# Optimization experiments

Hardware: AMD Instinct MI355X
Metric: run time of the kernel (lower is better)

The kernel has to match this reference:

```python
import jax, jax.numpy as jnp
import numpy as np

N_GROUPS = 32
EPS = 1e-5
N_HEADS = 8
D_K = 64


def setup_inputs() -> dict:
    key = jax.random.key(0)
    ks = jax.random.split(key, 4)
    B, C, H, W = 16, 512, 32, 32
    x = jax.random.normal(ks[0], (B, C, H, W), dtype=jnp.float32)
    gn_w = jnp.ones((C,), dtype=jnp.float32)
    gn_b = jnp.zeros((C,), dtype=jnp.float32)
    proj_w = jax.random.normal(ks[1], (3 * C, C), dtype=jnp.float32) * (C ** -0.5)
    proj_b = jnp.zeros((3 * C,), dtype=jnp.float32)
    out_w = jax.random.normal(ks[2], (C, C), dtype=jnp.float32) * (C ** -0.5)
    out_b = jnp.zeros((C,), dtype=jnp.float32)
    return {"x": x, "gn_w": gn_w, "gn_b": gn_b, "proj_w": proj_w,
            "proj_b": proj_b, "out_w": out_w, "out_b": out_b}


def _group_norm(x, w, b):
    B, C, H, W = x.shape
    xg = x.reshape(B, N_GROUPS, C // N_GROUPS, H, W)
    mean = xg.mean(axis=(2, 3, 4), keepdims=True)
    var = xg.var(axis=(2, 3, 4), keepdims=True)
    xn = (xg - mean) * jax.lax.rsqrt(var + EPS)
    xn = xn.reshape(B, C, H, W)
    return xn * w[None, :, None, None] + b[None, :, None, None]


def reference(x, gn_w, gn_b, proj_w, proj_b, out_w, out_b):
    B, C, H, W = x.shape
    S = H * W
    scale = D_K ** -0.25  # applied to both q and k, as in the original
    h = _group_norm(x, gn_w, gn_b).reshape(B, C, S).transpose(0, 2, 1)  # [B,S,C]
    qkv = h @ proj_w.T + proj_b  # [B,S,3C]
    qkv = qkv.reshape(B, S, N_HEADS, 3 * D_K)
    q, k, v = jnp.split(qkv, 3, axis=-1)  # each [B,S,H,D]
    attn = jnp.einsum('bihd,bjhd->bijh', q * scale, k * scale)  # [B,S,S,Hd]
    attn = jax.nn.softmax(attn, axis=2)
    res = jnp.einsum('bijh,bjhd->bihd', attn, v).reshape(B, S, N_HEADS * D_K)
    res = res @ out_w.T + out_b  # [B,S,C]
    res = res.transpose(0, 2, 1).reshape(B, C, H, W)
    return res + x
```

## Files before the change

### kernel.cpp

```cpp
#include <hip/hip_runtime.h>
#include <stdint.h>

typedef unsigned short u16;
typedef __attribute__((ext_vector_type(8))) short bf16x8;
typedef __attribute__((ext_vector_type(4))) short bf16x4;
typedef __attribute__((ext_vector_type(4))) float f32x4;
typedef __attribute__((ext_vector_type(4))) unsigned short u16x4;

#define GLD16(gp, lp) __builtin_amdgcn_global_load_lds( \
    (__attribute__((address_space(1))) void*)(void*)(gp), \
    (__attribute__((address_space(3))) void*)(void*)(lp), 16, 0, 0)

__device__ __forceinline__ u16 f2b(float f) {
  union { float f; unsigned u; } v; v.f = f;
  unsigned r = v.u + 0x7FFFu + ((v.u >> 16) & 1u);
  return (u16)(r >> 16);
}

__device__ __forceinline__ float fexp2(float x) {
#if __has_builtin(__builtin_amdgcn_exp2f)
  return __builtin_amdgcn_exp2f(x);
#else
  return exp2f(x);
#endif
}

__global__ __launch_bounds__(256) void gncvt_kernel(const float* __restrict__ x,
                                                    const float* __restrict__ gw,
                                                    const float* __restrict__ gb,
                                                    u16* __restrict__ h,
                                                    const float* __restrict__ wq_f,
                                                    const float* __restrict__ wo_f,
                                                    u16* __restrict__ wq,
                                                    u16* __restrict__ wo) {
  if (blockIdx.x >= 512) {
    int i = (blockIdx.x - 512) * 256 + threadIdx.x;
    const float* src; u16* dst; int j;
    if (i < 196608) { src = wq_f; dst = wq; j = i; }
    else            { src = wo_f; dst = wo; j = i - 196608; }
    const float4 f = ((const float4*)src)[j];
    u16x4 r; r[0] = f2b(f.x); r[1] = f2b(f.y); r[2] = f2b(f.z); r[3] = f2b(f.w);
    *(u16x4*)(dst + (size_t)j * 4) = r;
    return;
  }
  const int b = blockIdx.x >> 5, g = blockIdx.x & 31;
  const float* xg = x + ((size_t)(b * 512 + g * 16)) * 1024;
  const int tid = threadIdx.x;
  float4 vals[16];
  float s = 0.f, ss = 0.f;
#pragma unroll
  for (int j = 0; j < 16; j++) {
    const float4 v = ((const float4*)xg)[j * 256 + tid];
    vals[j] = v;
    s  += (v.x + v.y) + (v.z + v.w);
    ss += (v.x * v.x + v.y * v.y) + (v.z * v.z + v.w * v.w);
  }
#pragma unroll
  for (int off = 32; off; off >>= 1) { s += __shfl_down(s, off); ss += __shfl_down(ss, off); }
  __shared__ float red[8];
  const int wid = tid >> 6, lane = tid & 63;
  if (lane == 0) { red[wid] = s; red[4 + wid] = ss; }
  __syncthreads();
  if (tid == 0) {
    float S = red[0] + red[1] + red[2] + red[3];
    float SS = red[4] + red[5] + red[6] + red[7];
    float mean = S * (1.f / 16384.f);
    float var = SS * (1.f / 16384.f) - mean * mean;
    red[0] = mean; red[1] = rsqrtf(var + 1e-5f);
  }
  __syncthreads();
  const float mean = red[0], rs = red[1];
  float sc[16], bi[16];
#pragma unroll
  for (int c = 0; c < 16; c++) { sc[c] = gw[g * 16 + c] * rs; bi[c] = gb[g * 16 + c]; }
  u16* dst = h + ((size_t)(b * 32 + g) * 1024 + 4 * tid) * 16;
#pragma unroll
  for (int e = 0; e < 4; e++) {
    u16 row[16];
#pragma unroll
    for (int j = 0; j < 16; j++) {
      const float v = (e == 0) ? vals[j].x : (e == 1) ? vals[j].y : (e == 2) ? vals[j].z : vals[j].w;
      row[j] = f2b((v - mean) * sc[j] + bi[j]);
    }
    *(bf16x8*)(dst + e * 16) = *(bf16x8*)&row[0];
    *(bf16x8*)(dst + e * 16 + 8) = *(bf16x8*)&row[8];
  }
}

__global__ __launch_bounds__(512, 2) void qkv_gemm(const u16* __restrict__ h,
                                                   const u16* __restrict__ w,
                                                   const float* __restrict__ bias,
                                                   u16* __restrict__ q,
                                                   u16* __restrict__ k,
                                                   u16* __restrict__ v) {
  __shared__ u16 As[2][256 * 64];
  __shared__ u16 Bs[2][256 * 64];
  const int bm = blockIdx.x;
  const int bn = blockIdx.y;
  const int tid = threadIdx.x, lane = tid & 63, wid = tid >> 6;
  const int wm = wid & 1, wn = wid >> 1;
  const int c15 = lane & 15, quad = lane >> 4;
  const int sw = c15 & 7;
  const int b = bm >> 2;
  const int sp0 = (bm & 3) * 256;

  const int t8 = tid >> 3;
  const int lc = (tid & 7) ^ (t8 & 7);
  const u16* pA = h + (size_t)b * 524288 + (size_t)(lc >> 1) * 16384
                + (size_t)(sp0 + t8) * 16 + (lc & 1) * 8;
  const u16* pB = w + (size_t)(bn * 256 + t8) * 512 + lc * 8;

  const f32x4 fz = {0.f, 0.f, 0.f, 0.f};
  f32x4 acc[8][4];
#pragma unroll
  for (int i = 0; i < 8; i++)
#pragma unroll
    for (int j = 0; j < 4; j++) acc[i][j] = fz;

#pragma unroll
  for (int i = 0; i < 4; i++) {
    GLD16(pA + (size_t)i * 1024, &As[0][(i * 512 + tid) * 8]);
    GLD16(pB + (size_t)i * 32768, &Bs[0][(i * 512 + tid) * 8]);
  }
  asm volatile("s_waitcnt vmcnt(0)" ::: "memory");
  __builtin_amdgcn_s_barrier();
  __builtin_amdgcn_sched_barrier(0);

  for (int kt = 0; kt < 8; ++kt) {
    const int cb = kt & 1, db = cb ^ 1;
    if (kt < 7) {
#pragma unroll
      for (int i = 0; i < 4; i++) {
        GLD16(pA + (size_t)(kt + 1) * 65536 + (size_t)i * 1024, &As[db][(i * 512 + tid) * 8]);
        GLD16(pB + (size_t)(kt + 1) * 64 + (size_t)i * 32768, &Bs[db][(i * 512 + tid) * 8]);
      }
      __builtin_amdgcn_sched_barrier(0);
    }
    bf16x8 bfx[2][4];
#pragma unroll
    for (int kk = 0; kk < 2; kk++) {
      const int kc = ((kk * 4 + quad) ^ sw) * 8;
#pragma unroll
      for (int ni = 0; ni < 4; ni++)
        bfx[kk][ni] = *(const bf16x8*)&Bs[cb][(wn * 64 + ni * 16 + c15) * 64 + kc];
    }
#pragma unroll
    for (int ph = 0; ph < 2; ph++) {
      bf16x8 af[2][4];
#pragma unroll
      for (int kk = 0; kk < 2; kk++) {
        const int kc = ((kk * 4 + quad) ^ sw) * 8;
#pragma unroll
        for (int mi = 0; mi < 4; mi++)
          af[kk][mi] = *(const bf16x8*)&As[cb][(wm * 128 + ph * 64 + mi * 16 + c15) * 64 + kc];
      }
      __builtin_amdgcn_s_setprio(1);
#pragma unroll
      for (int kk = 0; kk < 2; kk++)
#pragma unroll
        for (int mi = 0; mi < 4; mi++)
#pragma unroll
          for (int ni = 0; ni < 4; ni++)
            acc[ph * 4 + mi][ni] = __builtin_amdgcn_mfma_f32_16x16x32_bf16(af[kk][mi], bfx[kk][ni], acc[ph * 4 + mi][ni], 0, 0, 0);
      __builtin_amdgcn_s_setprio(0);
    }
    asm volatile("s_waitcnt vmcnt(0)" ::: "memory");
    __builtin_amdgcn_s_barrier();
    __builtin_amdgcn_sched_barrier(0);
  }

  const float qscale = 0.51006972f;
  const float kscale = 0.35355339059327373f;
  const int quad4 = quad << 2;
#pragma unroll
  for (int mi = 0; mi < 8; mi++) {
    const int sp = sp0 + wm * 128 + mi * 16 + quad4;
#pragma unroll
    for (int ni = 0; ni < 4; ni++) {
      const int n = bn * 256 + wn * 64 + ni * 16 + c15;
      const int head = n / 192;
      const int rr = n - head * 192;
      const float bi = bias[n];
      const int d = rr & 63;
      if (rr < 128) {
        u16* dst = (rr < 64) ? q : k;
        const float sc = (rr < 64) ? qscale : kscale;
        dst += ((size_t)(b * 8 + head) * 1024 + sp) * 64 + d;
#pragma unroll
        for (int r = 0; r < 4; r++)
          dst[(size_t)r * 64] = f2b((acc[mi][ni][r] + bi) * sc);
      } else {
        u16x4 pk;
#pragma unroll
        for (int r = 0; r < 4; r++) pk[r] = f2b(acc[mi][ni][r] + bi);
        *(u16x4*)(v + ((size_t)(b * 8 + head) * 64 + d) * 1024 + sp) = pk;
      }
    }
  }
}

__global__ __launch_bounds__(512) void attn_kernel(const u16* __restrict__ q,
                                                   const u16* __restrict__ k,
                                                   const u16* __restrict__ vT,
                                                   u16* __restrict__ o) {
  __shared__ u16 Ks[2][64 * 64];
  __shared__ u16 Vs[2][64 * 64];
  const int bh = blockIdx.x;
  const int qb = blockIdx.y;
  const int tid = threadIdx.x, lane = tid & 63, wid = tid >> 6;
  const u16* Q = q + (size_t)bh * 1024 * 64;
  const u16* K = k + (size_t)bh * 1024 * 64;
  const u16* V = vT + (size_t)bh * 64 * 1024;
  const int qrow0 = qb * 256 + wid * 32;
  const int c15 = lane & 15, quad = lane >> 4;
  const int sw = c15 & 7;
  const int srow = tid >> 3;
  const int u8g  = tid & 7;
  const int s7 = srow & 7;
  const int kld = srow * 64 + ((u8g ^ s7) * 8);
  const int ve = 4 * (u8g >> 2) + 2 * (u8g & 1);
  const int vc = ((u8g >> 1) & 1) * 4;
  const int vld0 = srow * 64 + ((ve ^ s7) * 8) + vc;
  const int vld1 = srow * 64 + (((ve + 1) ^ s7) * 8) + vc;

  bf16x8 qf[2][2];
#pragma unroll
  for (int kk = 0; kk < 2; kk++)
#pragma unroll
    for (int ni = 0; ni < 2; ni++)
      qf[kk][ni] = *(const bf16x8*)(Q + (size_t)(qrow0 + ni * 16 + c15) * 64 + kk * 32 + quad * 8);

  const f32x4 fz = {0.f, 0.f, 0.f, 0.f};
  const float Mshift = 14.4269504089f;
  const f32x4 fm = {-Mshift, -Mshift, -Mshift, -Mshift};
  f32x4 oaccT[4][2];
#pragma unroll
  for (int i = 0; i < 4; i++)
#pragma unroll
    for (int j = 0; j < 2; j++) oaccT[i][j] = fz;
  float lsum[2] = {0.f, 0.f};

  bf16x8 kr, vr;
  kr = *(const bf16x8*)(K + (size_t)srow * 64 + u8g * 8);
  vr = *(const bf16x8*)(V + (size_t)srow * 1024 + u8g * 8);
  {
    u16* Kd = Ks[0]; u16* Vd = Vs[0];
    *(bf16x8*)&Kd[kld] = kr;
    union { bf16x4 h[2]; bf16x8 v; } a; a.v = vr;
    *(bf16x4*)&Vd[vld0] = a.h[0];
    *(bf16x4*)&Vd[vld1] = a.h[1];
  }
  kr = *(const bf16x8*)(K + (size_t)(64 + srow) * 64 + u8g * 8);
  vr = *(const bf16x8*)(V + (size_t)srow * 1024 + 64 + u8g * 8);

  for (int kt = 0; kt < 16; ++kt) {
    __syncthreads();
    const int cur = kt & 1, alt = cur ^ 1;
    if (kt < 15) {
      u16* Kd = Ks[alt]; u16* Vd = Vs[alt];
      *(bf16x8*)&Kd[kld] = kr;
      union { bf16x4 h[2]; bf16x8 v; } a; a.v = vr;
      *(bf16x4*)&Vd[vld0] = a.h[0];
      *(bf16x4*)&Vd[vld1] = a.h[1];
      const int pk2 = (kt + 2) & 15;
      kr = *(const bf16x8*)(K + ((size_t)pk2 * 64 + srow) * 64 + u8g * 8);
      vr = *(const bf16x8*)(V + (size_t)srow * 1024 + pk2 * 64 + u8g * 8);
    }
    const u16* Kc = Ks[cur];
    const u16* Vc = Vs[cur];

    f32x4 sacc[4][2];
#pragma unroll
    for (int i = 0; i < 4; i++)
#pragma unroll
      for (int j = 0; j < 2; j++) sacc[i][j] = fm;
#pragma unroll
    for (int kk = 0; kk < 2; kk++) {
      bf16x8 af[4];
#pragma unroll
      for (int mi = 0; mi < 4; mi++)
        af[mi] = *(const bf16x8*)&Kc[(mi * 16 + c15) * 64 + (((kk * 4 + quad) ^ sw) * 8)];
      __builtin_amdgcn_s_setprio(1);
#pragma unroll
      for (int mi = 0; mi < 4; mi++)
#pragma unroll
        for (int ni = 0; ni < 2; ni++)
          sacc[mi][ni] = __builtin_amdgcn_mfma_f32_16x16x32_bf16(af[mi], qf[kk][ni], sacc[mi][ni], 0, 0, 0);
      __builtin_amdgcn_s_setprio(0);
    }

    unsigned pkd[4][2][2];
#pragma unroll
    for (int ni = 0; ni < 2; ni++) {
      float ls = 0.f;
#pragma unroll
      for (int mi = 0; mi < 4; mi++) {
        unsigned pu[4];
#pragma unroll
        for (int r = 0; r < 4; r++) {
          const float p = fexp2(sacc[mi][ni][r]);
          ls += p;
          union { float f; unsigned u; } c; c.f = p;
          pu[r] = c.u;
        }
        pkd[mi][ni][0] = __builtin_amdgcn_perm(pu[1], pu[0], 0x07060302u);
        pkd[mi][ni][1] = __builtin_amdgcn_perm(pu[3], pu[2], 0x07060302u);
      }
      lsum[ni] += ls;
    }

#pragma unroll
    for (int mg = 0; mg < 2; mg++) {
      union { unsigned u[4]; bf16x8 v; } bb[2];
#pragma unroll
      for (int ni = 0; ni < 2; ni++) {
        bb[ni].u[0] = pkd[2 * mg][ni][0];     bb[ni].u[1] = pkd[2 * mg][ni][1];
        bb[ni].u[2] = pkd[2 * mg + 1][ni][0]; bb[ni].u[3] = pkd[2 * mg + 1][ni][1];
      }
      bf16x8 aa[4];
#pragma unroll
      for (int nd = 0; nd < 4; nd++)
        aa[nd] = *(const bf16x8*)&Vc[(nd * 16 + c15) * 64 + (((mg * 4 + quad) ^ sw) * 8)];
      __builtin_amdgcn_s_setprio(1);
#pragma unroll
      for (int nd = 0; nd < 4; nd++)
#pragma unroll
        for (int ni = 0; ni < 2; ni++)
          oaccT[nd][ni] = __builtin_amdgcn_mfma_f32_16x16x32_bf16(aa[nd], bb[ni].v, oaccT[nd][ni], 0, 0, 0);
      __builtin_amdgcn_s_setprio(0);
    }
  }

  float iv[2];
#pragma unroll
  for (int ni = 0; ni < 2; ni++) {
    float l = lsum[ni];
    l += __shfl_xor(l, 16);
    l += __shfl_xor(l, 32);
    iv[ni] = 1.f / l;
  }
  const int b = bh >> 3, hh = bh & 7;
#pragma unroll
  for (int ni = 0; ni < 2; ni++) {
    const int row = qrow0 + ni * 16 + c15;
#pragma unroll
    for (int nd = 0; nd < 4; nd++) {
      u16x4 pk4;
#pragma unroll
      for (int r = 0; r < 4; r++) pk4[r] = f2b(oaccT[nd][ni][r] * iv[ni]);
      *(u16x4*)(o + ((size_t)b * 1024 + row) * 512 + hh * 64 + nd * 16 + quad * 4) = pk4;
    }
  }
}

__global__ __launch_bounds__(256) void out_gemm(const u16* __restrict__ attn,
                                                const u16* __restrict__ wo,
                                                const float* __restrict__ ob,
                                                const float* __restrict__ x,
                                                float* __restrict__ out) {
  __shared__ u16 As[128 * 32];
  __shared__ u16 Bs[128 * 32];
  const int b = blockIdx.z;
  const int bm = blockIdx.x;
  const int bn = blockIdx.y;
  const int tid = threadIdx.x, lane = tid & 63, wid = tid >> 6;
  const int wm = wid & 1, wn = wid >> 1;
  const u16* gA = attn + ((size_t)b * 1024 + bm * 128) * 512;
  const u16* gB = wo + (size_t)bn * 128 * 512;

  const f32x4 fz = {0.f, 0.f, 0.f, 0.f};
  f32x4 acc[4][4];
#pragma unroll
  for (int i = 0; i < 4; i++)
#pragma unroll
    for (int j = 0; j < 4; j++) acc[i][j] = fz;

  const int r0 = lane >> 2;
  const int ch8 = (lane & 3) * 8;

  for (int kt = 0; kt < 16; ++kt) {
    __syncthreads();
#pragma unroll
    for (int j = 0; j < 2; ++j) {
      const int idx = wid * 2 + j;
      const int row = idx * 16 + r0;
      GLD16(gA + (size_t)row * 512 + kt * 32 + ch8, &As[idx * 512 + lane * 8]);
      GLD16(gB + (size_t)row * 512 + kt * 32 + ch8, &Bs[idx * 512 + lane * 8]);
    }
    __syncthreads();
    bf16x8 af[4], bf[4];
#pragma unroll
    for (int mi = 0; mi < 4; mi++)
      af[mi] = *(const bf16x8*)&As[(wm * 64 + mi * 16 + (lane & 15)) * 32 + (lane >> 4) * 8];
#pragma unroll
    for (int ni = 0; ni < 4; ni++)
      bf[ni] = *(const bf16x8*)&Bs[(wn * 64 + ni * 16 + (lane & 15)) * 32 + (lane >> 4) * 8];
#pragma unroll
    for (int mi = 0; mi < 4; mi++)
#pragma unroll
      for (int ni = 0; ni < 4; ni++)
        acc[mi][ni] = __builtin_amdgcn_mfma_f32_16x16x32_bf16(af[mi], bf[ni], acc[mi][ni], 0, 0, 0);
  }

  const int quad4 = (lane >> 4) << 2;
  const int c15_ = lane & 15;
#pragma unroll
  for (int mi = 0; mi < 4; mi++) {
    const int m = bm * 128 + wm * 64 + mi * 16 + quad4;
#pragma unroll
    for (int ni = 0; ni < 4; ni++) {
      const int c = bn * 128 + wn * 64 + ni * 16 + c15_;
      const float bo = ob[c];
      const size_t idx = ((size_t)b * 512 + c) * 1024 + m;
      const float4 xv = *(const float4*)(x + idx);
      float4 ov;
      ov.x = acc[mi][ni][0] + bo + xv.x;
      ov.y = acc[mi][ni][1] + bo + xv.y;
      ov.z = acc[mi][ni][2] + bo + xv.z;
      ov.w = acc[mi][ni][3] + bo + xv.w;
      *(float4*)(out + idx) = ov;
    }
  }
}

extern "C" void kernel_launch(void* const* d_in, const int* in_sizes, int n_in,
                              void* d_out, int out_size, void* d_ws, size_t ws_size,
                              hipStream_t stream) {
  const float* x      = (const float*)d_in[0];
  const float* gn_w   = (const float*)d_in[1];
  const float* gn_b   = (const float*)d_in[2];
  const float* proj_w = (const float*)d_in[3];
  const float* proj_b = (const float*)d_in[4];
  const float* out_w  = (const float*)d_in[5];
  const float* out_b  = (const float*)d_in[6];
  float* out = (float*)d_out;

  char* p = (char*)d_ws;
  u16* h    = (u16*)p; p += (size_t)16 * 1024 * 512 * 2;
  u16* q    = (u16*)p; p += (size_t)16 * 8 * 1024 * 64 * 2;
  u16* k    = (u16*)p; p += (size_t)16 * 8 * 1024 * 64 * 2;
  u16* v    = (u16*)p; p += (size_t)16 * 8 * 1024 * 64 * 2;
  u16* attn = (u16*)p; p += (size_t)16 * 1024 * 512 * 2;
  u16* wq   = (u16*)p; p += (size_t)1536 * 512 * 2;
  u16* wo   = (u16*)p; p += (size_t)512 * 512 * 2;

  gncvt_kernel<<<1536, 256, 0, stream>>>(x, gn_w, gn_b, h, proj_w, out_w, wq, wo);
  qkv_gemm<<<dim3(64, 6), 512, 0, stream>>>(h, wq, proj_b, q, k, v);
  attn_kernel<<<dim3(128, 4), 512, 0, stream>>>(q, k, v, attn);
  out_gemm<<<dim3(8, 4, 16), 256, 0, stream>>>(attn, wo, out_b, x, out);
}
```

Before: 204.1 us.

## Pre-tile h and QKV weights into swizzled K-tiles; shrink QKV GEMM tile for occupancy

The group-norm kernel and the weight conversion now write h and the projection weights directly in a pre-tiled, XOR-swizzled [tile][32-wide K] layout, so each GEMM K-step can be loaded with contiguous 16-byte global-to-LDS copies. The QKV GEMM tile drops from 256x256x64 to 256x96x32, which uses far less LDS, allows 4 blocks per CU, and raises the grid from 384 to 1024 blocks to fill the GPU better. The cost is lower per-block data reuse, more K iterations with a barrier each, and 16 rather than 8 pipeline steps.

```diff
diff --git a/kernel.cpp b/kernel.cpp
--- a/kernel.cpp
+++ b/kernel.cpp
@@ -24,6 +24,7 @@
   return exp2f(x);
 #endif
 }
+
 
 __global__ __launch_bounds__(256) void gncvt_kernel(const float* __restrict__ x,
                                                     const float* __restrict__ gw,
@@ -35,12 +36,20 @@
                                                     u16* __restrict__ wo) {
   if (blockIdx.x >= 512) {
     int i = (blockIdx.x - 512) * 256 + threadIdx.x;
-    const float* src; u16* dst; int j;
-    if (i < 196608) { src = wq_f; dst = wq; j = i; }
-    else            { src = wo_f; dst = wo; j = i - 196608; }
-    const float4 f = ((const float4*)src)[j];
-    u16x4 r; r[0] = f2b(f.x); r[1] = f2b(f.y); r[2] = f2b(f.z); r[3] = f2b(f.w);
-    *(u16x4*)(dst + (size_t)j * 4) = r;
+    if (i < 196608) {
+      const float4 f = ((const float4*)wq_f)[i];
+      const int n = i >> 7, c0 = (i & 127) * 4;
+      const int nt = n / 96, r = n - nt * 96;
+      const int kt = c0 >> 5, c8 = (c0 >> 3) & 3, wi = c0 & 7;
+      const int sel = (r >> 1) & 3;
+      u16x4 rr; rr[0] = f2b(f.x); rr[1] = f2b(f.y); rr[2] = f2b(f.z); rr[3] = f2b(f.w);
+      *(u16x4*)(wq + (size_t)(nt * 16 + kt) * 3072 + r * 32 + ((c8 ^ sel) * 8) + wi) = rr;
+    } else {
+      int j = i - 196608;
+      const float4 f = ((const float4*)wo_f)[j];
+      u16x4 rr; rr[0] = f2b(f.x); rr[1] = f2b(f.y); rr[2] = f2b(f.z); rr[3] = f2b(f.w);
+      *(u16x4*)(wo + (size_t)j * 4) = rr;
+    }
     return;
   }
   const int b = blockIdx.x >> 5, g = blockIdx.x & 31;
@@ -73,97 +82,80 @@
   float sc[16], bi[16];
 #pragma unroll
   for (int c = 0; c < 16; c++) { sc[c] = gw[g * 16 + c] * rs; bi[c] = gb[g * 16 + c]; }
-  u16* dst = h + ((size_t)(b * 32 + g) * 1024 + 4 * tid) * 16;
+  const int mt = b * 4 + (tid >> 6);
+  const int kt = g >> 1, c8a = (g & 1) * 2;
+  u16* base = h + (size_t)(mt * 16 + kt) * 8192;
 #pragma unroll
   for (int e = 0; e < 4; e++) {
+    const int r = (tid & 63) * 4 + e;
+    const int sel = (r >> 1) & 3;
     u16 row[16];
 #pragma unroll
     for (int j = 0; j < 16; j++) {
       const float v = (e == 0) ? vals[j].x : (e == 1) ? vals[j].y : (e == 2) ? vals[j].z : vals[j].w;
       row[j] = f2b((v - mean) * sc[j] + bi[j]);
     }
-    *(bf16x8*)(dst + e * 16) = *(bf16x8*)&row[0];
-    *(bf16x8*)(dst + e * 16 + 8) = *(bf16x8*)&row[8];
-  }
-}
-
-__global__ __launch_bounds__(512, 2) void qkv_gemm(const u16* __restrict__ h,
+    *(bf16x8*)(base + r * 32 + ((c8a ^ sel) * 8)) = *(bf16x8*)&row[0];
+    *(bf16x8*)(base + r * 32 + (((c8a + 1) ^ sel) * 8)) = *(bf16x8*)&row[8];
+  }
+}
+
+__global__ __launch_bounds__(512, 4) void qkv_gemm(const u16* __restrict__ h,
                                                    const u16* __restrict__ w,
                                                    const float* __restrict__ bias,
                                                    u16* __restrict__ q,
                                                    u16* __restrict__ k,
                                                    u16* __restrict__ v) {
-  __shared__ u16 As[2][256 * 64];
-  __shared__ u16 Bs[2][256 * 64];
+  __shared__ u16 As[2][8192];
+  __shared__ u16 Bs[2][3072];
   const int bm = blockIdx.x;
   const int bn = blockIdx.y;
   const int tid = threadIdx.x, lane = tid & 63, wid = tid >> 6;
-  const int wm = wid & 1, wn = wid >> 1;
+  const int wm = wid >> 1, wn = wid & 1;
   const int c15 = lane & 15, quad = lane >> 4;
-  const int sw = c15 & 7;
-  const int b = bm >> 2;
-  const int sp0 = (bm & 3) * 256;
-
-  const int t8 = tid >> 3;
-  const int lc = (tid & 7) ^ (t8 & 7);
-  const u16* pA = h + (size_t)b * 524288 + (size_t)(lc >> 1) * 16384
-                + (size_t)(sp0 + t8) * 16 + (lc & 1) * 8;
-  const u16* pB = w + (size_t)(bn * 256 + t8) * 512 + lc * 8;
+  const int kc = ((quad ^ ((c15 >> 1) & 3)) * 8);
+
+  const u16* pA = h + (size_t)bm * 16 * 8192 + (size_t)tid * 8;
+  const u16* pB = w + (size_t)bn * 16 * 3072 + (size_t)tid * 8;
+  const bool doB = (tid < 384);
 
   const f32x4 fz = {0.f, 0.f, 0.f, 0.f};
-  f32x4 acc[8][4];
-#pragma unroll
-  for (int i = 0; i < 8; i++)
-#pragma unroll
-    for (int j = 0; j < 4; j++) acc[i][j] = fz;
-
-#pragma unroll
-  for (int i = 0; i < 4; i++) {
-    GLD16(pA + (size_t)i * 1024, &As[0][(i * 512 + tid) * 8]);
-    GLD16(pB + (size_t)i * 32768, &Bs[0][(i * 512 + tid) * 8]);
-  }
+  f32x4 acc[4][3];
+#pragma unroll
+  for (int i = 0; i < 4; i++)
+#pragma unroll
+    for (int j = 0; j < 3; j++) acc[i][j] = fz;
+
+  GLD16(pA, &As[0][tid * 8]);
+  GLD16(pA + 4096, &As[0][4096 + tid * 8]);
+  if (doB) GLD16(pB, &Bs[0][tid * 8]);
   asm volatile("s_waitcnt vmcnt(0)" ::: "memory");
   __builtin_amdgcn_s_barrier();
   __builtin_amdgcn_sched_barrier(0);
 
-  for (int kt = 0; kt < 8; ++kt) {
+  for (int kt = 0; kt < 16; ++kt) {
     const int cb = kt & 1, db = cb ^ 1;
-    if (kt < 7) {
-#pragma unroll
-      for (int i = 0; i < 4; i++) {
-        GLD16(pA + (size_t)(kt + 1) * 65536 + (size_t)i * 1024, &As[db][(i * 512 + tid) * 8]);
-        GLD16(pB + (size_t)(kt + 1) * 64 + (size_t)i * 32768, &Bs[db][(i * 512 + tid) * 8]);
-      }
+    if (kt < 15) {
+      const u16* nA = pA + (size_t)(kt + 1) * 8192;
+      GLD16(nA, &As[db][tid * 8]);
+      GLD16(nA + 4096, &As[db][4096 + tid * 8]);
+      if (doB) GLD16(pB + (size_t)(kt + 1) * 3072, &Bs[db][tid * 8]);
       __builtin_amdgcn_sched_barrier(0);
     }
-    bf16x8 bfx[2][4];
-#pragma unroll
-    for (int kk = 0; kk < 2; kk++) {
-      const int kc = ((kk * 4 + quad) ^ sw) * 8;
-#pragma unroll
-      for (int ni = 0; ni < 4; ni++)
-        bfx[kk][ni] = *(const bf16x8*)&Bs[cb][(wn * 64 + ni * 16 + c15) * 64 + kc];
-    }
-#pragma unroll
-    for (int ph = 0; ph < 2; ph++) {
-      bf16x8 af[2][4];
-#pragma unroll
-      for (int kk = 0; kk < 2; kk++) {
-        const int kc = ((kk * 4 + quad) ^ sw) * 8;
-#pragma unroll
-        for (int mi = 0; mi < 4; mi++)
-          af[kk][mi] = *(const bf16x8*)&As[cb][(wm * 128 + ph * 64 + mi * 16 + c15) * 64 + kc];
-      }
-      __builtin_amdgcn_s_setprio(1);
-#pragma unroll
-      for (int kk = 0; kk < 2; kk++)
-#pragma unroll
-        for (int mi = 0; mi < 4; mi++)
-#pragma unroll
-          for (int ni = 0; ni < 4; ni++)
-            acc[ph * 4 + mi][ni] = __builtin_amdgcn_mfma_f32_16x16x32_bf16(af[kk][mi], bfx[kk][ni], acc[ph * 4 + mi][ni], 0, 0, 0);
-      __builtin_amdgcn_s_setprio(0);
-    }
+    bf16x8 af[4], bf[3];
+#pragma unroll
+    for (int mi = 0; mi < 4; mi++)
+      af[mi] = *(const bf16x8*)&As[cb][(wm * 64 + mi * 16 + c15) * 32 + kc];
+#pragma unroll
+    for (int ni = 0; ni < 3; ni++)
+      bf[ni] = *(const bf16x8*)&Bs[cb][(wn * 48 + ni * 16 + c15) * 32 + kc];
+    __builtin_amdgcn_s_setprio(1);
+#pragma unroll
+    for (int mi = 0; mi < 4; mi++)
+#pragma unroll
+      for (int ni = 0; ni < 3; ni++)
+        acc[mi][ni] = __builtin_amdgcn_mfma_f32_16x16x32_bf16(af[mi], bf[ni], acc[mi][ni], 0, 0, 0);
+    __builtin_amdgcn_s_setprio(0);
     asm volatile("s_waitcnt vmcnt(0)" ::: "memory");
     __builtin_amdgcn_s_barrier();
     __builtin_amdgcn_sched_barrier(0);
@@ -171,13 +163,14 @@
 
   const float qscale = 0.51006972f;
   const float kscale = 0.35355339059327373f;
+  const int b = bm >> 2;
   const int quad4 = quad << 2;
 #pragma unroll
-  for (int mi = 0; mi < 8; mi++) {
-    const int sp = sp0 + wm * 128 + mi * 16 + quad4;
-#pragma unroll
-    for (int ni = 0; ni < 4; ni++) {
-      const int n = bn * 256 + wn * 64 + ni * 16 + c15;
+  for (int mi = 0; mi < 4; mi++) {
+    const int sp = (bm & 3) * 256 + wm * 64 + mi * 16 + quad4;
+#pragma unroll
+    for (int ni = 0; ni < 3; ni++) {
+      const int n = bn * 96 + wn * 48 + ni * 16 + c15;
       const int head = n / 192;
       const int rr = n - head * 192;
       const float bi = bias[n];
@@ -445,7 +438,7 @@
   u16* wo   = (u16*)p; p += (size_t)512 * 512 * 2;
 
   gncvt_kernel<<<1536, 256, 0, stream>>>(x, gn_w, gn_b, h, proj_w, out_w, wq, wo);
-  qkv_gemm<<<dim3(64, 6), 512, 0, stream>>>(h, wq, proj_b, q, k, v);
+  qkv_gemm<<<dim3(64, 16), 512, 0, stream>>>(h, wq, proj_b, q, k, v);
   attn_kernel<<<dim3(128, 4), 512, 0, stream>>>(q, k, v, attn);
   out_gemm<<<dim3(8, 4, 16), 256, 0, stream>>>(attn, wo, out_b, x, out);
 }
```

New measurement: 195.8 us. 1.04x faster.

## Pre-tile h and Wqkv into LDS-ready swizzled blocks and interleave QKV GEMM phases

Applied to the files above, without the earlier changes.

The group-norm kernel and the weight-conversion path now write h and the QKV weight directly in a blocked, pre-swizzled tile layout. The GEMM can then load each 128x64 half-tile with contiguous 16-byte global-to-LDS copies. The QKV GEMM main loop is split into four MFMA phases, each separated by barriers, and the next tile's A/B loads are staged incrementally between phases with a partial vmcnt wait. This is meant to overlap global traffic with compute and simplify address math. The cost is extra barriers per k-step and a coupling of the layouts across kernels.

```diff
diff --git a/kernel.cpp b/kernel.cpp
--- a/kernel.cpp
+++ b/kernel.cpp
@@ -24,6 +24,7 @@
   return exp2f(x);
 #endif
 }
+
 
 __global__ __launch_bounds__(256) void gncvt_kernel(const float* __restrict__ x,
                                                     const float* __restrict__ gw,
@@ -35,12 +36,20 @@
                                                     u16* __restrict__ wo) {
   if (blockIdx.x >= 512) {
     int i = (blockIdx.x - 512) * 256 + threadIdx.x;
-    const float* src; u16* dst; int j;
-    if (i < 196608) { src = wq_f; dst = wq; j = i; }
-    else            { src = wo_f; dst = wo; j = i - 196608; }
-    const float4 f = ((const float4*)src)[j];
-    u16x4 r; r[0] = f2b(f.x); r[1] = f2b(f.y); r[2] = f2b(f.z); r[3] = f2b(f.w);
-    *(u16x4*)(dst + (size_t)j * 4) = r;
+    if (i < 196608) {
+      const float4 f = ((const float4*)wq_f)[i];
+      const int n = i >> 7, c0 = (i & 127) * 4;
+      const int bn = n >> 8, half = (n >> 7) & 1, r = n & 127;
+      const int kt = c0 >> 6, ch = (c0 >> 3) & 7, j = c0 & 7;
+      const int sel2 = ((r >> 2) & 1) << 1;
+      u16x4 rr; rr[0] = f2b(f.x); rr[1] = f2b(f.y); rr[2] = f2b(f.z); rr[3] = f2b(f.w);
+      *(u16x4*)(wq + ((size_t)(bn * 8 + kt) * 2 + half) * 8192 + r * 64 + ((ch ^ sel2) * 8) + j) = rr;
+    } else {
+      int j = i - 196608;
+      const float4 f = ((const float4*)wo_f)[j];
+      u16x4 rr; rr[0] = f2b(f.x); rr[1] = f2b(f.y); rr[2] = f2b(f.z); rr[3] = f2b(f.w);
+      *(u16x4*)(wo + (size_t)j * 4) = rr;
+    }
     return;
   }
   const int b = blockIdx.x >> 5, g = blockIdx.x & 31;
@@ -73,17 +82,23 @@
   float sc[16], bi[16];
 #pragma unroll
   for (int c = 0; c < 16; c++) { sc[c] = gw[g * 16 + c] * rs; bi[c] = gb[g * 16 + c]; }
-  u16* dst = h + ((size_t)(b * 32 + g) * 1024 + 4 * tid) * 16;
+  const int kt = g >> 2;
+  const int bmq = tid >> 6;
+  const int half = (tid >> 5) & 1;
+  const int sel2 = (tid & 1) << 1;
+  const int cph = (((g & 3) * 2) ^ sel2) * 8;
+  u16* base = h + ((size_t)((b * 4 + bmq) * 8 + kt) * 2 + half) * 8192;
 #pragma unroll
   for (int e = 0; e < 4; e++) {
+    const int r = (tid & 31) * 4 + e;
     u16 row[16];
 #pragma unroll
     for (int j = 0; j < 16; j++) {
       const float v = (e == 0) ? vals[j].x : (e == 1) ? vals[j].y : (e == 2) ? vals[j].z : vals[j].w;
       row[j] = f2b((v - mean) * sc[j] + bi[j]);
     }
-    *(bf16x8*)(dst + e * 16) = *(bf16x8*)&row[0];
-    *(bf16x8*)(dst + e * 16 + 8) = *(bf16x8*)&row[8];
+    *(bf16x8*)(base + r * 64 + cph) = *(bf16x8*)&row[0];
+    *(bf16x8*)(base + r * 64 + cph + 8) = *(bf16x8*)&row[8];
   }
 }
 
@@ -93,22 +108,21 @@
                                                    u16* __restrict__ q,
                                                    u16* __restrict__ k,
                                                    u16* __restrict__ v) {
-  __shared__ u16 As[2][256 * 64];
-  __shared__ u16 Bs[2][256 * 64];
+  __shared__ u16 As[2][16384];
+  __shared__ u16 Bs[2][16384];
   const int bm = blockIdx.x;
   const int bn = blockIdx.y;
   const int tid = threadIdx.x, lane = tid & 63, wid = tid >> 6;
-  const int wm = wid & 1, wn = wid >> 1;
+  const int wm = wid >> 2, wn = wid & 3;
   const int c15 = lane & 15, quad = lane >> 4;
-  const int sw = c15 & 7;
-  const int b = bm >> 2;
-  const int sp0 = (bm & 3) * 256;
-
-  const int t8 = tid >> 3;
-  const int lc = (tid & 7) ^ (t8 & 7);
-  const u16* pA = h + (size_t)b * 524288 + (size_t)(lc >> 1) * 16384
-                + (size_t)(sp0 + t8) * 16 + (lc & 1) * 8;
-  const u16* pB = w + (size_t)(bn * 256 + t8) * 512 + lc * 8;
+  const int sel2 = ((c15 >> 2) & 1) << 1;
+  const int ck0 = ((quad) ^ sel2) * 8;
+  const int ck1 = ((4 + quad) ^ sel2) * 8;
+  const u16* hA = h + (size_t)bm * 131072;
+  const u16* wB = w + (size_t)bn * 131072;
+
+  const int aBase = wm * 8192 + c15 * 64;
+  const int bBase = (wn >> 1) * 8192 + ((wn & 1) * 64 + c15) * 64;
 
   const f32x4 fz = {0.f, 0.f, 0.f, 0.f};
   f32x4 acc[8][4];
@@ -118,63 +132,119 @@
     for (int j = 0; j < 4; j++) acc[i][j] = fz;
 
 #pragma unroll
-  for (int i = 0; i < 4; i++) {
-    GLD16(pA + (size_t)i * 1024, &As[0][(i * 512 + tid) * 8]);
-    GLD16(pB + (size_t)i * 32768, &Bs[0][(i * 512 + tid) * 8]);
+  for (int ht = 0; ht < 2; ht++) {
+    GLD16(hA + ht * 8192 + tid * 8, &As[0][ht * 8192 + tid * 8]);
+    GLD16(hA + ht * 8192 + 4096 + tid * 8, &As[0][ht * 8192 + 4096 + tid * 8]);
+    GLD16(wB + ht * 8192 + tid * 8, &Bs[0][ht * 8192 + tid * 8]);
+    GLD16(wB + ht * 8192 + 4096 + tid * 8, &Bs[0][ht * 8192 + 4096 + tid * 8]);
   }
   asm volatile("s_waitcnt vmcnt(0)" ::: "memory");
   __builtin_amdgcn_s_barrier();
   __builtin_amdgcn_sched_barrier(0);
 
+#define STAGE_A(HT) { const u16* sp_ = hA + (size_t)(kt + 1) * 16384 + (HT) * 8192 + tid * 8; \
+    GLD16(sp_, &As[db][(HT) * 8192 + tid * 8]); \
+    GLD16(sp_ + 4096, &As[db][(HT) * 8192 + 4096 + tid * 8]); }
+#define STAGE_B(HT) { const u16* sp_ = wB + (size_t)(kt + 1) * 16384 + (HT) * 8192 + tid * 8; \
+    GLD16(sp_, &Bs[db][(HT) * 8192 + tid * 8]); \
+    GLD16(sp_ + 4096, &Bs[db][(HT) * 8192 + 4096 + tid * 8]); }
+#define PH_SYNC() { __builtin_amdgcn_s_barrier(); \
+    asm volatile("s_waitcnt lgkmcnt(0)" ::: "memory"); \
+    __builtin_amdgcn_sched_barrier(0); }
+#define PH_END() { __builtin_amdgcn_s_barrier(); __builtin_amdgcn_sched_barrier(0); }
+
   for (int kt = 0; kt < 8; ++kt) {
     const int cb = kt & 1, db = cb ^ 1;
-    if (kt < 7) {
-#pragma unroll
-      for (int i = 0; i < 4; i++) {
-        GLD16(pA + (size_t)(kt + 1) * 65536 + (size_t)i * 1024, &As[db][(i * 512 + tid) * 8]);
-        GLD16(pB + (size_t)(kt + 1) * 64 + (size_t)i * 32768, &Bs[db][(i * 512 + tid) * 8]);
-      }
-      __builtin_amdgcn_sched_barrier(0);
-    }
-    bf16x8 bfx[2][4];
-#pragma unroll
-    for (int kk = 0; kk < 2; kk++) {
-      const int kc = ((kk * 4 + quad) ^ sw) * 8;
-#pragma unroll
-      for (int ni = 0; ni < 4; ni++)
-        bfx[kk][ni] = *(const bf16x8*)&Bs[cb][(wn * 64 + ni * 16 + c15) * 64 + kc];
-    }
-#pragma unroll
-    for (int ph = 0; ph < 2; ph++) {
-      bf16x8 af[2][4];
-#pragma unroll
-      for (int kk = 0; kk < 2; kk++) {
-        const int kc = ((kk * 4 + quad) ^ sw) * 8;
-#pragma unroll
-        for (int mi = 0; mi < 4; mi++)
-          af[kk][mi] = *(const bf16x8*)&As[cb][(wm * 128 + ph * 64 + mi * 16 + c15) * 64 + kc];
-      }
-      __builtin_amdgcn_s_setprio(1);
-#pragma unroll
-      for (int kk = 0; kk < 2; kk++)
-#pragma unroll
-        for (int mi = 0; mi < 4; mi++)
-#pragma unroll
-          for (int ni = 0; ni < 4; ni++)
-            acc[ph * 4 + mi][ni] = __builtin_amdgcn_mfma_f32_16x16x32_bf16(af[kk][mi], bfx[kk][ni], acc[ph * 4 + mi][ni], 0, 0, 0);
-      __builtin_amdgcn_s_setprio(0);
-    }
-    asm volatile("s_waitcnt vmcnt(0)" ::: "memory");
-    __builtin_amdgcn_s_barrier();
-    __builtin_amdgcn_sched_barrier(0);
-  }
+    const bool st = (kt < 7);
+    bf16x8 af[2][4], bf01[2][2], bf23[2][2];
+
+#pragma unroll
+    for (int mi = 0; mi < 4; mi++) {
+      af[0][mi] = *(const bf16x8*)&As[cb][aBase + (mi * 16) * 64 + ck0];
+      af[1][mi] = *(const bf16x8*)&As[cb][aBase + (mi * 16) * 64 + ck1];
+    }
+#pragma unroll
+    for (int ni = 0; ni < 2; ni++) {
+      bf01[0][ni] = *(const bf16x8*)&Bs[cb][bBase + (ni * 16) * 64 + ck0];
+      bf01[1][ni] = *(const bf16x8*)&Bs[cb][bBase + (ni * 16) * 64 + ck1];
+    }
+    if (st) STAGE_A(0)
+    PH_SYNC();
+    __builtin_amdgcn_s_setprio(1);
+#pragma unroll
+    for (int kk = 0; kk < 2; kk++)
+#pragma unroll
+      for (int mi = 0; mi < 4; mi++)
+#pragma unroll
+        for (int ni = 0; ni < 2; ni++)
+          acc[mi][ni] = __builtin_amdgcn_mfma_f32_16x16x32_bf16(af[kk][mi], bf01[kk][ni], acc[mi][ni], 0, 0, 0);
+    __builtin_amdgcn_s_setprio(0);
+    PH_END();
+
+#pragma unroll
+    for (int ni = 0; ni < 2; ni++) {
+      bf23[0][ni] = *(const bf16x8*)&Bs[cb][bBase + ((2 + ni) * 16) * 64 + ck0];
+      bf23[1][ni] = *(const bf16x8*)&Bs[cb][bBase + ((2 + ni) * 16) * 64 + ck1];
+    }
+    if (st) STAGE_A(1)
+    PH_SYNC();
+    __builtin_amdgcn_s_setprio(1);
+#pragma unroll
+    for (int kk = 0; kk < 2; kk++)
+#pragma unroll
+      for (int mi = 0; mi < 4; mi++)
+#pragma unroll
+        for (int ni = 0; ni < 2; ni++)
+          acc[mi][2 + ni] = __builtin_amdgcn_mfma_f32_16x16x32_bf16(af[kk][mi], bf23[kk][ni], acc[mi][2 + ni], 0, 0, 0);
+    __builtin_amdgcn_s_setprio(0);
+    PH_END();
+
+#pragma unroll
+    for (int mi = 0; mi < 4; mi++) {
+      af[0][mi] = *(const bf16x8*)&As[cb][aBase + (64 + mi * 16) * 64 + ck0];
+      af[1][mi] = *(const bf16x8*)&As[cb][aBase + (64 + mi * 16) * 64 + ck1];
+    }
+    if (st) STAGE_B(0)
+    PH_SYNC();
+    __builtin_amdgcn_s_setprio(1);
+#pragma unroll
+    for (int kk = 0; kk < 2; kk++)
+#pragma unroll
+      for (int mi = 0; mi < 4; mi++)
+#pragma unroll
+        for (int ni = 0; ni < 2; ni++)
+          acc[4 + mi][2 + ni] = __builtin_amdgcn_mfma_f32_16x16x32_bf16(af[kk][mi], bf23[kk][ni], acc[4 + mi][2 + ni], 0, 0, 0);
+    __builtin_amdgcn_s_setprio(0);
+    PH_END();
+
+    if (st) {
+      STAGE_B(1)
+      asm volatile("s_waitcnt vmcnt(6)" ::: "memory");
+    }
+    PH_SYNC();
+    __builtin_amdgcn_s_setprio(1);
+#pragma unroll
+    for (int kk = 0; kk < 2; kk++)
+#pragma unroll
+      for (int mi = 0; mi < 4; mi++)
+#pragma unroll
+        for (int ni = 0; ni < 2; ni++)
+          acc[4 + mi][ni] = __builtin_amdgcn_mfma_f32_16x16x32_bf16(af[kk][mi], bf01[kk][ni], acc[4 + mi][ni], 0, 0, 0);
+    __builtin_amdgcn_s_setprio(0);
+    PH_END();
+  }
+#undef STAGE_A
+#undef STAGE_B
+#undef PH_SYNC
+#undef PH_END
 
   const float qscale = 0.51006972f;
   const float kscale = 0.35355339059327373f;
+  const int b = bm >> 2;
   const int quad4 = quad << 2;
 #pragma unroll
-  for (int mi = 0; mi < 8; mi++) {
-    const int sp = sp0 + wm * 128 + mi * 16 + quad4;
+  for (int a = 0; a < 8; a++) {
+    const int sp = (bm & 3) * 256 + wm * 128 + (a >> 2) * 64 + (a & 3) * 16 + quad4;
 #pragma unroll
     for (int ni = 0; ni < 4; ni++) {
       const int n = bn * 256 + wn * 64 + ni * 16 + c15;
@@ -188,11 +258,11 @@
         dst += ((size_t)(b * 8 + head) * 1024 + sp) * 64 + d;
 #pragma unroll
         for (int r = 0; r < 4; r++)
-          dst[(size_t)r * 64] = f2b((acc[mi][ni][r] + bi) * sc);
+          dst[(size_t)r * 64] = f2b((acc[a][ni][r] + bi) * sc);
       } else {
         u16x4 pk;
 #pragma unroll
-        for (int r = 0; r < 4; r++) pk[r] = f2b(acc[mi][ni][r] + bi);
+        for (int r = 0; r < 4; r++) pk[r] = f2b(acc[a][ni][r] + bi);
         *(u16x4*)(v + ((size_t)(b * 8 + head) * 64 + d) * 1024 + sp) = pk;
       }
     }
```

Result: slower. 211.6 us (+3.6%).
